# Performance work log

Measured on AMD Instinct MI355X. Metric: run time of the kernel, lower is better.

Reference implementation:

```python
import jax, jax.numpy as jnp
import numpy as np

B, T, N, E = 8, 32, 128, 2048
IN_DIM, HID, OUT = 512, 512, 512
SLOPE = 0.2  # GATConv default negative_slope


def setup_inputs() -> dict:
    key = jax.random.key(0)
    ks = jax.random.split(key, 12)
    x = jax.random.normal(ks[0], (B, T, N, IN_DIM), jnp.float32)
    edge_index = jax.random.randint(ks[1], (B, T, 2, E), 0, N)
    valid_step_index = jax.random.randint(ks[2], (B,), 1, T + 1)
    def lin(k, o, i):
        return jax.random.normal(k, (o, i), jnp.float32) / np.sqrt(i).astype(np.float32)
    W1 = lin(ks[3], HID, IN_DIM)
    a1_src = jax.random.normal(ks[4], (HID,), jnp.float32) / np.sqrt(HID).astype(np.float32)
    a1_dst = jax.random.normal(ks[5], (HID,), jnp.float32) / np.sqrt(HID).astype(np.float32)
    b1 = jnp.zeros((HID,), jnp.float32)
    W2 = lin(ks[6], OUT, HID)
    a2_src = jax.random.normal(ks[7], (OUT,), jnp.float32) / np.sqrt(OUT).astype(np.float32)
    a2_dst = jax.random.normal(ks[8], (OUT,), jnp.float32) / np.sqrt(OUT).astype(np.float32)
    b2 = jnp.zeros((OUT,), jnp.float32)
    W_time = jax.random.normal(ks[9], (T, T), jnp.float32) / np.sqrt(T).astype(np.float32)
    b_time = jnp.zeros((T,), jnp.float32)
    return dict(x=x, edge_index=edge_index, valid_step_index=valid_step_index,
                W1=W1, a1_src=a1_src, a1_dst=a1_dst, b1=b1,
                W2=W2, a2_src=a2_src, a2_dst=a2_dst, b2=b2,
                W_time=W_time, b_time=b_time)


def _gat(x, src, dst, W, a_src, a_dst, b):
    # Single-head PyG GATConv (concat=True, heads=1), self-loops already appended.
    n = x.shape[0]
    h = x @ W.T                                             # [N, H]
    e = jax.nn.leaky_relu((h @ a_src)[src] + (h @ a_dst)[dst], SLOPE)  # [E]
    m = jax.ops.segment_max(e, dst, num_segments=n)
    m = jnp.where(jnp.isfinite(m), m, 0.0)
    p = jnp.exp(e - m[dst])
    denom = jax.ops.segment_sum(p, dst, num_segments=n)
    alpha = p / denom[dst]                                  # segment softmax over incoming edges
    return jax.ops.segment_sum(h[src] * alpha[:, None], dst, num_segments=n) + b


def reference(x, edge_index, valid_step_index, W1, a1_src, a1_dst, b1,
              W2, a2_src, a2_dst, b2, W_time, b_time):
    b_, t_, n_, _ = x.shape
    g = b_ * t_
    xf = x.reshape(g, n_, -1)
    ei = edge_index.reshape(g, 2, -1)
    # add self loops (PyG GATConv default add_self_loops=True)
    loops = jnp.broadcast_to(jnp.arange(n_)[None, None, :], (g, 2, n_))
    ei = jnp.concatenate([ei, loops], axis=-1)
    src, dst = ei[:, 0], ei[:, 1]
    gat = jax.vmap(_gat, in_axes=(0, 0, 0, None, None, None, None))
    h = jax.nn.gelu(gat(xf, src, dst, W1, a1_src, a1_dst, b1), approximate=False)
    # F.dropout(p=0.2) is identity in eval mode
    h = gat(h, src, dst, W2, a2_src, a2_dst, b2)
    y = h.reshape(b_, t_, n_, -1)
    mask = (jnp.arange(t_)[None, :] < valid_step_index[:, None]).astype(y.dtype)
    y = y * mask[:, :, None, None]
    # TemporalConv: Conv2d(T, T, 1) over time-as-channel = linear mix across time, then GELU, residual
    fused = jax.nn.gelu(jnp.einsum('ts,bsnf->btnf', W_time, y)
                        + b_time[None, :, None, None], approximate=False)
    return fused + y
```

## Files before the change

kernel.cpp:

```cpp
#include <hip/hip_runtime.h>

using u16 = unsigned short;
using u32 = unsigned int;

typedef __bf16 bf16x8 __attribute__((ext_vector_type(8)));
typedef float  f32x4  __attribute__((ext_vector_type(4)));

__device__ __forceinline__ u16 f2bf(float f) {
    u32 u = __float_as_uint(f);
    u32 r = u + 0x7fffu + ((u >> 16) & 1u);
    return (u16)(r >> 16);
}
__device__ __forceinline__ float gelu_f(float x) {
    return 0.5f * x * (1.0f + erff(x * 0.70710678118654752440f));
}

#define GLOAD16(gp, lp) __builtin_amdgcn_global_load_lds( \
    (const __attribute__((address_space(1))) void*)(gp),  \
    (__attribute__((address_space(3))) void*)(lp), 16, 0, 0)
#define WAITV0  asm volatile("s_waitcnt vmcnt(0)" ::: "memory")
#define WAITL0  asm volatile("s_waitcnt lgkmcnt(0)" ::: "memory")
#define BARRIER __builtin_amdgcn_s_barrier()

__global__ __launch_bounds__(256) void prep_kernel(
    const float* __restrict__ W1, const float* __restrict__ W2,
    u16* __restrict__ W1b, u16* __restrict__ W2b)
{
    int i = blockIdx.x * 256 + threadIdx.x;
    const float* src = (i < 65536) ? W1 : W2;
    u16* dst = (i < 65536) ? W1b : W2b;
    int ii = i & 65535;
    int f = ii >> 7;
    int k = (ii & 127) * 4;
    float4 v = ((const float4*)src)[ii];
    int kd = (k & ~31) | ((((k >> 3) & 3) ^ (f & 3)) << 3) | (k & 7);
    ushort4 o;
    o.x = f2bf(v.x); o.y = f2bf(v.y); o.z = f2bf(v.z); o.w = f2bf(v.w);
    *(ushort4*)&dst[f * 512 + kd] = o;
}

__global__ __launch_bounds__(512, 2) void mega_kernel(
    const float* __restrict__ x, const int* __restrict__ ei, const int* __restrict__ valid,
    const u16* __restrict__ W1b, const float* __restrict__ a1s, const float* __restrict__ a1d,
    const float* __restrict__ b1,
    const u16* __restrict__ W2b, const float* __restrict__ a2s, const float* __restrict__ a2d,
    const float* __restrict__ b2,
    float* __restrict__ outF)
{
    __shared__ u16 Hs[65536];
    __shared__ __align__(16) u16 SG[16384];

    const int tid  = threadIdx.x;
    const int lane = tid & 63;
    const int w    = tid >> 6;
    const int rl   = lane & 15;
    const int grp  = lane >> 4;
    const int gid  = blockIdx.x;
    const int bb   = gid >> 5, tt = gid & 31;

    float* stf = (float*)(SG + 12288);
    u32*   cntw = (u32*)SG;
    const unsigned char* cb = (const unsigned char*)SG;

    const int xr = tid >> 2, xq = tid & 3;
    const float* xg = x + (size_t)gid * 65536;


    {
        f32x4 acc[8][4] = {};
        float4 xa = *(const float4*)(xg + xr * 512 + xq * 8);
        float4 xc = *(const float4*)(xg + xr * 512 + xq * 8 + 4);
        for (int kt = 0; kt < 16; ++kt) {
            {
                const u16* s0 = W1b + (size_t)(w * 64 + (lane >> 2)) * 512 + kt * 32 + (lane & 3) * 8;
                GLOAD16(s0,            &SG[4096 + w * 1024]);
                GLOAD16(s0 + 16 * 512, &SG[4096 + w * 1024 + 512]);
            }
            {
                ushort4 lo, hi;
                lo.x = f2bf(xa.x); lo.y = f2bf(xa.y); lo.z = f2bf(xa.z); lo.w = f2bf(xa.w);
                hi.x = f2bf(xc.x); hi.y = f2bf(xc.y); hi.z = f2bf(xc.z); hi.w = f2bf(xc.w);
                int xo = xr * 32 + ((xq ^ (xr & 3)) << 3);
                *(ushort4*)&SG[xo]     = lo;
                *(ushort4*)&SG[xo + 4] = hi;
            }
            WAITV0; BARRIER;
            bf16x8 af[8];
            #pragma unroll
            for (int i = 0; i < 8; ++i)
                af[i] = *(const bf16x8*)&SG[(i * 16 + rl) * 32 + ((grp ^ (rl & 3)) << 3)];
            bf16x8 bv0 = *(const bf16x8*)&SG[4096 + w * 1024 + (rl) * 32      + ((grp ^ (rl & 3)) << 3)];
            bf16x8 bv1 = *(const bf16x8*)&SG[4096 + w * 1024 + (16 + rl) * 32 + ((grp ^ (rl & 3)) << 3)];
            WAITL0; BARRIER;
            {
                const u16* s0 = W1b + (size_t)(w * 64 + 32 + (lane >> 2)) * 512 + kt * 32 + (lane & 3) * 8;
                GLOAD16(s0,            &SG[4096 + w * 1024]);
                GLOAD16(s0 + 16 * 512, &SG[4096 + w * 1024 + 512]);
            }
            #pragma unroll
            for (int i = 0; i < 8; ++i) {
                acc[i][0] = __builtin_amdgcn_mfma_f32_16x16x32_bf16(af[i], bv0, acc[i][0], 0, 0, 0);
                acc[i][1] = __builtin_amdgcn_mfma_f32_16x16x32_bf16(af[i], bv1, acc[i][1], 0, 0, 0);
            }
            WAITV0; BARRIER;
            bf16x8 bv2 = *(const bf16x8*)&SG[4096 + w * 1024 + (rl) * 32      + ((grp ^ (rl & 3)) << 3)];
            bf16x8 bv3 = *(const bf16x8*)&SG[4096 + w * 1024 + (16 + rl) * 32 + ((grp ^ (rl & 3)) << 3)];
            WAITL0;
            if (kt < 15) {
                xa = *(const float4*)(xg + xr * 512 + (kt + 1) * 32 + xq * 8);
                xc = *(const float4*)(xg + xr * 512 + (kt + 1) * 32 + xq * 8 + 4);
            }
            #pragma unroll
            for (int i = 0; i < 8; ++i) {
                acc[i][2] = __builtin_amdgcn_mfma_f32_16x16x32_bf16(af[i], bv2, acc[i][2], 0, 0, 0);
                acc[i][3] = __builtin_amdgcn_mfma_f32_16x16x32_bf16(af[i], bv3, acc[i][3], 0, 0, 0);
            }
            BARRIER;
        }
        stf[tid] = 0.f;
        __syncthreads();
        float asv[4], adv[4];
        #pragma unroll
        for (int j = 0; j < 4; ++j) {
            int f = w * 64 + j * 16 + rl;
            asv[j] = a1s[f]; adv[j] = a1d[f];
        }
        #pragma unroll
        for (int i = 0; i < 8; ++i) {
            #pragma unroll
            for (int j = 0; j < 4; ++j) {
                int f = w * 64 + j * 16 + rl;
                ushort4 o;
                o.x = f2bf(acc[i][j][0]); o.y = f2bf(acc[i][j][1]);
                o.z = f2bf(acc[i][j][2]); o.w = f2bf(acc[i][j][3]);
                *(ushort4*)&Hs[(f * 128 + i * 16 + grp * 4) ^ ((f & 7) << 3)] = o;
            }
            #pragma unroll
            for (int r = 0; r < 4; ++r) {
                float s = acc[i][0][r] * asv[0] + acc[i][1][r] * asv[1]
                        + acc[i][2][r] * asv[2] + acc[i][3][r] * asv[3];
                float d = acc[i][0][r] * adv[0] + acc[i][1][r] * adv[1]
                        + acc[i][2][r] * adv[2] + acc[i][3][r] * adv[3];
                #pragma unroll
                for (int off = 1; off < 16; off <<= 1) {
                    s += __shfl_xor(s, off);
                    d += __shfl_xor(d, off);
                }
                if (rl == 0) {
                    atomicAdd(&stf[i * 16 + grp * 4 + r], s);
                    atomicAdd(&stf[128 + i * 16 + grp * 4 + r], d);
                }
            }
        }
        __syncthreads();
    }

    {
        for (int i = tid; i < 4096; i += 512) cntw[i] = 0u;
        __syncthreads();
        const int4* es = (const int4*)(ei + (size_t)gid * 4096);
        int4 s4 = es[tid], d4 = es[512 + tid];
        atomicAdd(&cntw[(u32)((d4.x * 32 + (s4.x >> 2)) ^ ((d4.x & 7) << 1))], 1u << (8 * (s4.x & 3)));
        atomicAdd(&cntw[(u32)((d4.y * 32 + (s4.y >> 2)) ^ ((d4.y & 7) << 1))], 1u << (8 * (s4.y & 3)));
        atomicAdd(&cntw[(u32)((d4.z * 32 + (s4.z >> 2)) ^ ((d4.z & 7) << 1))], 1u << (8 * (s4.z & 3)));
        atomicAdd(&cntw[(u32)((d4.w * 32 + (s4.w >> 2)) ^ ((d4.w & 7) << 1))], 1u << (8 * (s4.w & 3)));
        if (tid < 128)
            atomicAdd(&cntw[(u32)((tid * 32 + (tid >> 2)) ^ ((tid & 7) << 1))], 1u << (8 * (tid & 3)));
        __syncthreads();
        for (int r = 0; r < 16; ++r) {
            int m = w * 16 + r;
            float sdm = stf[128 + m];
            int s0 = lane, s1 = lane + 64;
            u32 c0 = cb[((m * 128 + (s0 & ~3)) ^ ((m & 7) << 3)) + (s0 & 3)];
            u32 c1 = cb[((m * 128 + (s1 & ~3)) ^ ((m & 7) << 3)) + (s1 & 3)];
            float e0 = stf[s0] + sdm; e0 = e0 > 0.f ? e0 : 0.2f * e0;
            float e1 = stf[s1] + sdm; e1 = e1 > 0.f ? e1 : 0.2f * e1;
            float mx = fmaxf(c0 ? e0 : -1e30f, c1 ? e1 : -1e30f);
            #pragma unroll
            for (int off = 1; off < 64; off <<= 1) mx = fmaxf(mx, __shfl_xor(mx, off));
            float p = (c0 ? (float)c0 * __expf(e0 - mx) : 0.f)
                    + (c1 ? (float)c1 * __expf(e1 - mx) : 0.f);
            #pragma unroll
            for (int off = 1; off < 64; off <<= 1) p += __shfl_xor(p, off);
            if (lane == 0) { stf[256 + m] = mx; stf[384 + m] = 1.f / p; }
        }
        __syncthreads();
    }

    {
        f32x4 acc2[32] = {};
        int m = w * 16 + rl;
        float Mm = stf[256 + m], rDm = stf[384 + m], sdm = stf[128 + m];
        bf16x8 pa[4];
        #pragma unroll
        for (int kb = 0; kb < 4; ++kb) {
            u32 wi = (u32)((m * 32 + kb * 8 + grp * 2) ^ ((m & 7) << 1));
            u32 w0 = cntw[wi], w1 = cntw[wi + 1];
            #pragma unroll
            for (int e = 0; e < 8; ++e) {
                int s = kb * 32 + grp * 8 + e;
                u32 c = ((e < 4 ? (w0 >> (8 * e)) : (w1 >> (8 * (e - 4)))) & 255u);
                float ev = stf[s] + sdm; ev = ev > 0.f ? ev : 0.2f * ev;
                float p = c ? (float)c * __expf(ev - Mm) * rDm : 0.f;
                pa[kb][e] = (__bf16)p;
            }
        }
        #pragma unroll
        for (int j = 0; j < 32; ++j) {
            int f = j * 16 + rl;
            #pragma unroll
            for (int kb = 0; kb < 4; ++kb) {
                bf16x8 hb = *(const bf16x8*)&Hs[(f * 128 + kb * 32 + grp * 8) ^ ((f & 7) << 3)];
                acc2[j] = __builtin_amdgcn_mfma_f32_16x16x32_bf16(pa[kb], hb, acc2[j], 0, 0, 0);
            }
        }
        __syncthreads();
        #pragma unroll
        for (int j = 0; j < 32; ++j) {
            int f = j * 16 + rl;
            float bv = b1[f];
            #pragma unroll
            for (int r = 0; r < 4; ++r) {
                int mm = w * 16 + grp * 4 + r;
                Hs[(mm * 512 + f) ^ ((mm & 7) << 3)] = f2bf(gelu_f(acc2[j][r] + bv));
            }
        }
        __syncthreads();
    }

    {
        f32x4 acc[8][4] = {};
        for (int kt = 0; kt < 16; ++kt) {
            {
                const u16* s0 = W2b + (size_t)(w * 64 + (lane >> 2)) * 512 + kt * 32 + (lane & 3) * 8;
                GLOAD16(s0,            &SG[4096 + w * 1024]);
                GLOAD16(s0 + 16 * 512, &SG[4096 + w * 1024 + 512]);
            }
            WAITV0; BARRIER;
            bf16x8 af[8];
            #pragma unroll
            for (int i = 0; i < 8; ++i)
                af[i] = *(const bf16x8*)&Hs[((i * 16 + rl) * 512 + kt * 32 + grp * 8) ^ ((rl & 7) << 3)];
            bf16x8 bv0 = *(const bf16x8*)&SG[4096 + w * 1024 + (rl) * 32      + ((grp ^ (rl & 3)) << 3)];
            bf16x8 bv1 = *(const bf16x8*)&SG[4096 + w * 1024 + (16 + rl) * 32 + ((grp ^ (rl & 3)) << 3)];
            WAITL0; BARRIER;
            {
                const u16* s0 = W2b + (size_t)(w * 64 + 32 + (lane >> 2)) * 512 + kt * 32 + (lane & 3) * 8;
                GLOAD16(s0,            &SG[4096 + w * 1024]);
                GLOAD16(s0 + 16 * 512, &SG[4096 + w * 1024 + 512]);
            }
            #pragma unroll
            for (int i = 0; i < 8; ++i) {
                acc[i][0] = __builtin_amdgcn_mfma_f32_16x16x32_bf16(af[i], bv0, acc[i][0], 0, 0, 0);
                acc[i][1] = __builtin_amdgcn_mfma_f32_16x16x32_bf16(af[i], bv1, acc[i][1], 0, 0, 0);
            }
            WAITV0; BARRIER;
            bf16x8 bv2 = *(const bf16x8*)&SG[4096 + w * 1024 + (rl) * 32      + ((grp ^ (rl & 3)) << 3)];
            bf16x8 bv3 = *(const bf16x8*)&SG[4096 + w * 1024 + (16 + rl) * 32 + ((grp ^ (rl & 3)) << 3)];
            WAITL0;
            #pragma unroll
            for (int i = 0; i < 8; ++i) {
                acc[i][2] = __builtin_amdgcn_mfma_f32_16x16x32_bf16(af[i], bv2, acc[i][2], 0, 0, 0);
                acc[i][3] = __builtin_amdgcn_mfma_f32_16x16x32_bf16(af[i], bv3, acc[i][3], 0, 0, 0);
            }
            BARRIER;
        }
        stf[tid] = 0.f;
        __syncthreads();
        float asv[4], adv[4];
        #pragma unroll
        for (int j = 0; j < 4; ++j) {
            int f = w * 64 + j * 16 + rl;
            asv[j] = a2s[f]; adv[j] = a2d[f];
        }
        #pragma unroll
        for (int i = 0; i < 8; ++i) {
            #pragma unroll
            for (int j = 0; j < 4; ++j) {
                int f = w * 64 + j * 16 + rl;
                ushort4 o;
                o.x = f2bf(acc[i][j][0]); o.y = f2bf(acc[i][j][1]);
                o.z = f2bf(acc[i][j][2]); o.w = f2bf(acc[i][j][3]);
                *(ushort4*)&Hs[(f * 128 + i * 16 + grp * 4) ^ ((f & 7) << 3)] = o;
            }
            #pragma unroll
            for (int r = 0; r < 4; ++r) {
                float s = acc[i][0][r] * asv[0] + acc[i][1][r] * asv[1]
                        + acc[i][2][r] * asv[2] + acc[i][3][r] * asv[3];
                float d = acc[i][0][r] * adv[0] + acc[i][1][r] * adv[1]
                        + acc[i][2][r] * adv[2] + acc[i][3][r] * adv[3];
                #pragma unroll
                for (int off = 1; off < 16; off <<= 1) {
                    s += __shfl_xor(s, off);
                    d += __shfl_xor(d, off);
                }
                if (rl == 0) {
                    atomicAdd(&stf[i * 16 + grp * 4 + r], s);
                    atomicAdd(&stf[128 + i * 16 + grp * 4 + r], d);
                }
            }
        }
        __syncthreads();
    }

    {
        for (int i = tid; i < 4096; i += 512) cntw[i] = 0u;
        __syncthreads();
        const int4* es = (const int4*)(ei + (size_t)gid * 4096);
        int4 s4 = es[tid], d4 = es[512 + tid];
        atomicAdd(&cntw[(u32)((d4.x * 32 + (s4.x >> 2)) ^ ((d4.x & 7) << 1))], 1u << (8 * (s4.x & 3)));
        atomicAdd(&cntw[(u32)((d4.y * 32 + (s4.y >> 2)) ^ ((d4.y & 7) << 1))], 1u << (8 * (s4.y & 3)));
        atomicAdd(&cntw[(u32)((d4.z * 32 + (s4.z >> 2)) ^ ((d4.z & 7) << 1))], 1u << (8 * (s4.z & 3)));
        atomicAdd(&cntw[(u32)((d4.w * 32 + (s4.w >> 2)) ^ ((d4.w & 7) << 1))], 1u << (8 * (s4.w & 3)));
        if (tid < 128)
            atomicAdd(&cntw[(u32)((tid * 32 + (tid >> 2)) ^ ((tid & 7) << 1))], 1u << (8 * (tid & 3)));
        __syncthreads();
        for (int r = 0; r < 16; ++r) {
            int m = w * 16 + r;
            float sdm = stf[128 + m];
            int s0 = lane, s1 = lane + 64;
            u32 c0 = cb[((m * 128 + (s0 & ~3)) ^ ((m & 7) << 3)) + (s0 & 3)];
            u32 c1 = cb[((m * 128 + (s1 & ~3)) ^ ((m & 7) << 3)) + (s1 & 3)];
            float e0 = stf[s0] + sdm; e0 = e0 > 0.f ? e0 : 0.2f * e0;
            float e1 = stf[s1] + sdm; e1 = e1 > 0.f ? e1 : 0.2f * e1;
            float mx = fmaxf(c0 ? e0 : -1e30f, c1 ? e1 : -1e30f);
            #pragma unroll
            for (int off = 1; off < 64; off <<= 1) mx = fmaxf(mx, __shfl_xor(mx, off));
            float p = (c0 ? (float)c0 * __expf(e0 - mx) : 0.f)
                    + (c1 ? (float)c1 * __expf(e1 - mx) : 0.f);
            #pragma unroll
            for (int off = 1; off < 64; off <<= 1) p += __shfl_xor(p, off);
            if (lane == 0) { stf[256 + m] = mx; stf[384 + m] = 1.f / p; }
        }
        __syncthreads();
    }

    {
        f32x4 acc2[32] = {};
        int m = w * 16 + rl;
        float Mm = stf[256 + m], rDm = stf[384 + m], sdm = stf[128 + m];
        bf16x8 pa[4];
        #pragma unroll
        for (int kb = 0; kb < 4; ++kb) {
            u32 wi = (u32)((m * 32 + kb * 8 + grp * 2) ^ ((m & 7) << 1));
            u32 w0 = cntw[wi], w1 = cntw[wi + 1];
            #pragma unroll
            for (int e = 0; e < 8; ++e) {
                int s = kb * 32 + grp * 8 + e;
                u32 c = ((e < 4 ? (w0 >> (8 * e)) : (w1 >> (8 * (e - 4)))) & 255u);
                float ev = stf[s] + sdm; ev = ev > 0.f ? ev : 0.2f * ev;
                float p = c ? (float)c * __expf(ev - Mm) * rDm : 0.f;
                pa[kb][e] = (__bf16)p;
            }
        }
        #pragma unroll
        for (int j = 0; j < 32; ++j) {
            int f = j * 16 + rl;
            #pragma unroll
            for (int kb = 0; kb < 4; ++kb) {
                bf16x8 hb = *(const bf16x8*)&Hs[(f * 128 + kb * 32 + grp * 8) ^ ((f & 7) << 3)];
                acc2[j] = __builtin_amdgcn_mfma_f32_16x16x32_bf16(pa[kb], hb, acc2[j], 0, 0, 0);
            }
        }
        float msk = (tt < valid[bb]) ? 1.f : 0.f;
        float* og = outF + (size_t)gid * 65536;
        #pragma unroll
        for (int j = 0; j < 32; ++j) {
            int g = j * 16 + rl;
            float bv = b2[g];
            #pragma unroll
            for (int r = 0; r < 4; ++r)
                og[(w * 16 + grp * 4 + r) * 512 + g] = (acc2[j][r] + bv) * msk;
        }
    }
}

__global__ __launch_bounds__(256) void timemix_kernel(float* __restrict__ y,
                                                      const float* __restrict__ Wt,
                                                      const float* __restrict__ bt) {
    __shared__ float wsm[1024];
    __shared__ float bts[32];
    int tid = threadIdx.x;
    for (int i = tid; i < 1024; i += 256) wsm[i] = Wt[i];
    if (tid < 32) bts[tid] = bt[tid];
    __syncthreads();
    int blk = blockIdx.x;
    int b = blk >> 8;
    int rem = blk & 255;
    int n = rem >> 1;
    int f = (rem & 1) * 256 + tid;
    size_t base = ((size_t)b * 4096 + n) * 512 + f;
    float ys[32];
    #pragma unroll
    for (int s = 0; s < 32; ++s) ys[s] = y[base + (size_t)s * 65536];
    #pragma unroll
    for (int t = 0; t < 32; ++t) {
        float a = bts[t];
        #pragma unroll
        for (int s = 0; s < 32; ++s) a += wsm[t * 32 + s] * ys[s];
        y[base + (size_t)t * 65536] = gelu_f(a) + ys[t];
    }
}

extern "C" void kernel_launch(void* const* d_in, const int* in_sizes, int n_in,
                              void* d_out, int out_size, void* d_ws, size_t ws_size,
                              hipStream_t stream) {
    const float* x     = (const float*)d_in[0];
    const int*   ei    = (const int*)d_in[1];
    const int*   valid = (const int*)d_in[2];
    const float* W1    = (const float*)d_in[3];
    const float* a1s   = (const float*)d_in[4];
    const float* a1d   = (const float*)d_in[5];
    const float* b1    = (const float*)d_in[6];
    const float* W2    = (const float*)d_in[7];
    const float* a2s   = (const float*)d_in[8];
    const float* a2d   = (const float*)d_in[9];
    const float* b2    = (const float*)d_in[10];
    const float* Wt    = (const float*)d_in[11];
    const float* bt    = (const float*)d_in[12];
    float* out = (float*)d_out;

    char* ws = (char*)d_ws;
    u16* W1b = (u16*)(ws);
    u16* W2b = (u16*)(ws + 524288);

    prep_kernel<<<512, 256, 0, stream>>>(W1, W2, W1b, W2b);
    mega_kernel<<<256, 512, 0, stream>>>(x, ei, valid,
        W1b, a1s, a1d, b1, W2b, a2s, a2d, b2, out);
    timemix_kernel<<<2048, 256, 0, stream>>>(out, Wt, bt);
}
```

Measured before the change: 198.9 us.

## Stage x into LDS upfront, pipeline W loads per-wave, share adjacency across layers

Converts the whole x tile to bf16 into LDS once instead of per k-step, and replaces the barrier-heavy W staging with a per-wave double-buffered ring that uses vmcnt(1) waits. The goal is to overlap global loads with MFMA and drop block-wide barriers from the GEMM loop. The edge-count adjacency is built once with 4-bit packed counts and reused by both GAT layers, which are now folded into one loop. The 4-bit counts cap duplicate edges per pair at 15, and the new swizzles change LDS access patterns.

Measured after the change: 218.1 us. 1.1x slower.

```diff
diff --git a/kernel.cpp b/kernel.cpp
--- a/kernel.cpp
+++ b/kernel.cpp
@@ -18,9 +18,8 @@
 #define GLOAD16(gp, lp) __builtin_amdgcn_global_load_lds( \
     (const __attribute__((address_space(1))) void*)(gp),  \
     (__attribute__((address_space(3))) void*)(lp), 16, 0, 0)
-#define WAITV0  asm volatile("s_waitcnt vmcnt(0)" ::: "memory")
-#define WAITL0  asm volatile("s_waitcnt lgkmcnt(0)" ::: "memory")
-#define BARRIER __builtin_amdgcn_s_barrier()
+#define WAITV(n) asm volatile("s_waitcnt vmcnt(" #n ")" ::: "memory")
+#define WAITL0   asm volatile("s_waitcnt lgkmcnt(0)" ::: "memory")
 
 __global__ __launch_bounds__(256) void prep_kernel(
     const float* __restrict__ W1, const float* __restrict__ W2,
@@ -49,6 +48,9 @@
 {
     __shared__ u16 Hs[65536];
     __shared__ __align__(16) u16 SG[16384];
+    u32*   cntw = (u32*)SG;
+    u16*   ring = SG + 4096;
+    float* stf  = (float*)(SG + 12288);
 
     const int tid  = threadIdx.x;
     const int lane = tid & 63;
@@ -58,319 +60,191 @@
     const int gid  = blockIdx.x;
     const int bb   = gid >> 5, tt = gid & 31;
 
-    float* stf = (float*)(SG + 12288);
-    u32*   cntw = (u32*)SG;
-    const unsigned char* cb = (const unsigned char*)SG;
-
-    const int xr = tid >> 2, xq = tid & 3;
-    const float* xg = x + (size_t)gid * 65536;
-
-
-    {
+    const int4* es = (const int4*)(ei + (size_t)gid * 4096);
+    int4 e0 = es[tid], e1 = es[512 + tid];
+
+    for (int i = tid; i < 2048; i += 512) cntw[i] = 0u;
+    stf[tid] = 0.f;
+
+    const float4* xg = (const float4*)(x + (size_t)gid * 65536);
+    #pragma unroll
+    for (int it = 0; it < 16; ++it) {
+        float4 a = xg[tid * 2 + it * 1024];
+        float4 b = xg[tid * 2 + 1 + it * 1024];
+        int m = it * 8 + w;
+        int sp = lane ^ ((lane >> 3) & 7) ^ (m & 7);
+        ushort4 lo, hi;
+        lo.x = f2bf(a.x); lo.y = f2bf(a.y); lo.z = f2bf(a.z); lo.w = f2bf(a.w);
+        hi.x = f2bf(b.x); hi.y = f2bf(b.y); hi.z = f2bf(b.z); hi.w = f2bf(b.w);
+        *(ushort4*)&Hs[m * 512 + sp * 8]     = lo;
+        *(ushort4*)&Hs[m * 512 + sp * 8 + 4] = hi;
+    }
+    __syncthreads();
+
+    atomicAdd(&cntw[e1.x * 16 + (e0.x >> 3)], 1u << ((e0.x & 7) * 4));
+    atomicAdd(&cntw[e1.y * 16 + (e0.y >> 3)], 1u << ((e0.y & 7) * 4));
+    atomicAdd(&cntw[e1.z * 16 + (e0.z >> 3)], 1u << ((e0.z & 7) * 4));
+    atomicAdd(&cntw[e1.w * 16 + (e0.w >> 3)], 1u << ((e0.w & 7) * 4));
+    if (tid < 128) atomicAdd(&cntw[tid * 16 + (tid >> 3)], 1u << ((tid & 7) * 4));
+    __syncthreads();
+
+    u16* myring = ring + w * 1024;
+
+    for (int L = 0; L < 2; ++L) {
+        const u16*  WL  = L ? W2b : W1b;
+        const float* av_s = L ? a2s : a1s;
+        const float* av_d = L ? a2d : a1d;
+
         f32x4 acc[8][4] = {};
-        float4 xa = *(const float4*)(xg + xr * 512 + xq * 8);
-        float4 xc = *(const float4*)(xg + xr * 512 + xq * 8 + 4);
-        for (int kt = 0; kt < 16; ++kt) {
-            {
-                const u16* s0 = W1b + (size_t)(w * 64 + (lane >> 2)) * 512 + kt * 32 + (lane & 3) * 8;
-                GLOAD16(s0,            &SG[4096 + w * 1024]);
-                GLOAD16(s0 + 16 * 512, &SG[4096 + w * 1024 + 512]);
-            }
-            {
-                ushort4 lo, hi;
-                lo.x = f2bf(xa.x); lo.y = f2bf(xa.y); lo.z = f2bf(xa.z); lo.w = f2bf(xa.w);
-                hi.x = f2bf(xc.x); hi.y = f2bf(xc.y); hi.z = f2bf(xc.z); hi.w = f2bf(xc.w);
-                int xo = xr * 32 + ((xq ^ (xr & 3)) << 3);
-                *(ushort4*)&SG[xo]     = lo;
-                *(ushort4*)&SG[xo + 4] = hi;
-            }
-            WAITV0; BARRIER;
-            bf16x8 af[8];
-            #pragma unroll
-            for (int i = 0; i < 8; ++i)
-                af[i] = *(const bf16x8*)&SG[(i * 16 + rl) * 32 + ((grp ^ (rl & 3)) << 3)];
-            bf16x8 bv0 = *(const bf16x8*)&SG[4096 + w * 1024 + (rl) * 32      + ((grp ^ (rl & 3)) << 3)];
-            bf16x8 bv1 = *(const bf16x8*)&SG[4096 + w * 1024 + (16 + rl) * 32 + ((grp ^ (rl & 3)) << 3)];
-            WAITL0; BARRIER;
-            {
-                const u16* s0 = W1b + (size_t)(w * 64 + 32 + (lane >> 2)) * 512 + kt * 32 + (lane & 3) * 8;
-                GLOAD16(s0,            &SG[4096 + w * 1024]);
-                GLOAD16(s0 + 16 * 512, &SG[4096 + w * 1024 + 512]);
-            }
-            #pragma unroll
-            for (int i = 0; i < 8; ++i) {
-                acc[i][0] = __builtin_amdgcn_mfma_f32_16x16x32_bf16(af[i], bv0, acc[i][0], 0, 0, 0);
-                acc[i][1] = __builtin_amdgcn_mfma_f32_16x16x32_bf16(af[i], bv1, acc[i][1], 0, 0, 0);
-            }
-            WAITV0; BARRIER;
-            bf16x8 bv2 = *(const bf16x8*)&SG[4096 + w * 1024 + (rl) * 32      + ((grp ^ (rl & 3)) << 3)];
-            bf16x8 bv3 = *(const bf16x8*)&SG[4096 + w * 1024 + (16 + rl) * 32 + ((grp ^ (rl & 3)) << 3)];
-            WAITL0;
-            if (kt < 15) {
-                xa = *(const float4*)(xg + xr * 512 + (kt + 1) * 32 + xq * 8);
-                xc = *(const float4*)(xg + xr * 512 + (kt + 1) * 32 + xq * 8 + 4);
-            }
-            #pragma unroll
-            for (int i = 0; i < 8; ++i) {
-                acc[i][2] = __builtin_amdgcn_mfma_f32_16x16x32_bf16(af[i], bv2, acc[i][2], 0, 0, 0);
-                acc[i][3] = __builtin_amdgcn_mfma_f32_16x16x32_bf16(af[i], bv3, acc[i][3], 0, 0, 0);
-            }
-            BARRIER;
-        }
-        stf[tid] = 0.f;
+        {
+            auto STAGEW = [&](int q) {
+                int kt2 = q >> 2, j2 = q & 3;
+                const u16* src = WL + (size_t)(w * 64 + j2 * 16 + (lane >> 2)) * 512
+                               + kt2 * 32 + (lane & 3) * 8;
+                GLOAD16(src, &myring[(q & 1) * 512]);
+            };
+            STAGEW(0); STAGEW(1);
+            for (int kt = 0; kt < 16; ++kt) {
+                bf16x8 af[8];
+                #pragma unroll
+                for (int i = 0; i < 8; ++i) {
+                    int m = i * 16 + rl;
+                    int sp = (kt * 4 + grp) ^ (kt >> 1) ^ (m & 7);
+                    af[i] = *(const bf16x8*)&Hs[m * 512 + sp * 8];
+                }
+                #pragma unroll
+                for (int j = 0; j < 4; ++j) {
+                    int q = kt * 4 + j;
+                    if (kt == 15 && j == 3) { WAITV(0); } else { WAITV(1); }
+                    bf16x8 bv = *(const bf16x8*)&myring[(q & 1) * 512 + rl * 32 + ((grp ^ (rl & 3)) * 8)];
+                    WAITL0;
+                    __builtin_amdgcn_sched_barrier(0);
+                    if (q + 2 < 64) STAGEW(q + 2);
+                    #pragma unroll
+                    for (int i = 0; i < 8; ++i)
+                        acc[i][j] = __builtin_amdgcn_mfma_f32_16x16x32_bf16(af[i], bv, acc[i][j], 0, 0, 0);
+                }
+            }
+        }
         __syncthreads();
-        float asv[4], adv[4];
-        #pragma unroll
-        for (int j = 0; j < 4; ++j) {
-            int f = w * 64 + j * 16 + rl;
-            asv[j] = a1s[f]; adv[j] = a1d[f];
-        }
-        #pragma unroll
-        for (int i = 0; i < 8; ++i) {
+
+        {
+            float asv[4], adv[4];
             #pragma unroll
             for (int j = 0; j < 4; ++j) {
                 int f = w * 64 + j * 16 + rl;
-                ushort4 o;
-                o.x = f2bf(acc[i][j][0]); o.y = f2bf(acc[i][j][1]);
-                o.z = f2bf(acc[i][j][2]); o.w = f2bf(acc[i][j][3]);
-                *(ushort4*)&Hs[(f * 128 + i * 16 + grp * 4) ^ ((f & 7) << 3)] = o;
-            }
-            #pragma unroll
-            for (int r = 0; r < 4; ++r) {
-                float s = acc[i][0][r] * asv[0] + acc[i][1][r] * asv[1]
-                        + acc[i][2][r] * asv[2] + acc[i][3][r] * asv[3];
-                float d = acc[i][0][r] * adv[0] + acc[i][1][r] * adv[1]
-                        + acc[i][2][r] * adv[2] + acc[i][3][r] * adv[3];
-                #pragma unroll
-                for (int off = 1; off < 16; off <<= 1) {
-                    s += __shfl_xor(s, off);
-                    d += __shfl_xor(d, off);
-                }
-                if (rl == 0) {
-                    atomicAdd(&stf[i * 16 + grp * 4 + r], s);
-                    atomicAdd(&stf[128 + i * 16 + grp * 4 + r], d);
+                asv[j] = av_s[f]; adv[j] = av_d[f];
+            }
+            #pragma unroll
+            for (int i = 0; i < 8; ++i) {
+                #pragma unroll
+                for (int j = 0; j < 4; ++j) {
+                    int f = j * 16 + rl + w * 64;
+                    int oct = i * 2 + (grp >> 1);
+                    int elem = f * 128 + ((oct ^ (f & 15)) * 8) + (grp & 1) * 4;
+                    ushort4 o;
+                    o.x = f2bf(acc[i][j][0]); o.y = f2bf(acc[i][j][1]);
+                    o.z = f2bf(acc[i][j][2]); o.w = f2bf(acc[i][j][3]);
+                    *(ushort4*)&Hs[elem] = o;
+                }
+                #pragma unroll
+                for (int r = 0; r < 4; ++r) {
+                    float s = acc[i][0][r] * asv[0] + acc[i][1][r] * asv[1]
+                            + acc[i][2][r] * asv[2] + acc[i][3][r] * asv[3];
+                    float d = acc[i][0][r] * adv[0] + acc[i][1][r] * adv[1]
+                            + acc[i][2][r] * adv[2] + acc[i][3][r] * adv[3];
+                    #pragma unroll
+                    for (int off = 1; off < 16; off <<= 1) {
+                        s += __shfl_xor(s, off);
+                        d += __shfl_xor(d, off);
+                    }
+                    if (rl == 0) {
+                        int m = i * 16 + grp * 4 + r;
+                        atomicAdd(&stf[m], s);
+                        atomicAdd(&stf[128 + m], d);
+                    }
                 }
             }
         }
         __syncthreads();
-    }
-
-    {
-        for (int i = tid; i < 4096; i += 512) cntw[i] = 0u;
-        __syncthreads();
-        const int4* es = (const int4*)(ei + (size_t)gid * 4096);
-        int4 s4 = es[tid], d4 = es[512 + tid];
-        atomicAdd(&cntw[(u32)((d4.x * 32 + (s4.x >> 2)) ^ ((d4.x & 7) << 1))], 1u << (8 * (s4.x & 3)));
-        atomicAdd(&cntw[(u32)((d4.y * 32 + (s4.y >> 2)) ^ ((d4.y & 7) << 1))], 1u << (8 * (s4.y & 3)));
-        atomicAdd(&cntw[(u32)((d4.z * 32 + (s4.z >> 2)) ^ ((d4.z & 7) << 1))], 1u << (8 * (s4.z & 3)));
-        atomicAdd(&cntw[(u32)((d4.w * 32 + (s4.w >> 2)) ^ ((d4.w & 7) << 1))], 1u << (8 * (s4.w & 3)));
-        if (tid < 128)
-            atomicAdd(&cntw[(u32)((tid * 32 + (tid >> 2)) ^ ((tid & 7) << 1))], 1u << (8 * (tid & 3)));
-        __syncthreads();
+
         for (int r = 0; r < 16; ++r) {
             int m = w * 16 + r;
             float sdm = stf[128 + m];
-            int s0 = lane, s1 = lane + 64;
-            u32 c0 = cb[((m * 128 + (s0 & ~3)) ^ ((m & 7) << 3)) + (s0 & 3)];
-            u32 c1 = cb[((m * 128 + (s1 & ~3)) ^ ((m & 7) << 3)) + (s1 & 3)];
-            float e0 = stf[s0] + sdm; e0 = e0 > 0.f ? e0 : 0.2f * e0;
-            float e1 = stf[s1] + sdm; e1 = e1 > 0.f ? e1 : 0.2f * e1;
-            float mx = fmaxf(c0 ? e0 : -1e30f, c1 ? e1 : -1e30f);
+            u32 w0 = cntw[m * 16 + (lane >> 3)];
+            u32 w1 = cntw[m * 16 + 8 + (lane >> 3)];
+            u32 c0 = (w0 >> ((lane & 7) * 4)) & 15u;
+            u32 c1 = (w1 >> ((lane & 7) * 4)) & 15u;
+            float E0 = stf[lane] + sdm;      E0 = E0 > 0.f ? E0 : 0.2f * E0;
+            float E1 = stf[lane + 64] + sdm; E1 = E1 > 0.f ? E1 : 0.2f * E1;
+            float mx = fmaxf(c0 ? E0 : -1e30f, c1 ? E1 : -1e30f);
             #pragma unroll
             for (int off = 1; off < 64; off <<= 1) mx = fmaxf(mx, __shfl_xor(mx, off));
-            float p = (c0 ? (float)c0 * __expf(e0 - mx) : 0.f)
-                    + (c1 ? (float)c1 * __expf(e1 - mx) : 0.f);
+            float p = (c0 ? (float)c0 * __expf(E0 - mx) : 0.f)
+                    + (c1 ? (float)c1 * __expf(E1 - mx) : 0.f);
             #pragma unroll
             for (int off = 1; off < 64; off <<= 1) p += __shfl_xor(p, off);
             if (lane == 0) { stf[256 + m] = mx; stf[384 + m] = 1.f / p; }
         }
         __syncthreads();
-    }
-
-    {
+
         f32x4 acc2[32] = {};
-        int m = w * 16 + rl;
-        float Mm = stf[256 + m], rDm = stf[384 + m], sdm = stf[128 + m];
-        bf16x8 pa[4];
-        #pragma unroll
-        for (int kb = 0; kb < 4; ++kb) {
-            u32 wi = (u32)((m * 32 + kb * 8 + grp * 2) ^ ((m & 7) << 1));
-            u32 w0 = cntw[wi], w1 = cntw[wi + 1];
-            #pragma unroll
-            for (int e = 0; e < 8; ++e) {
-                int s = kb * 32 + grp * 8 + e;
-                u32 c = ((e < 4 ? (w0 >> (8 * e)) : (w1 >> (8 * (e - 4)))) & 255u);
-                float ev = stf[s] + sdm; ev = ev > 0.f ? ev : 0.2f * ev;
-                float p = c ? (float)c * __expf(ev - Mm) * rDm : 0.f;
-                pa[kb][e] = (__bf16)p;
-            }
-        }
-        #pragma unroll
-        for (int j = 0; j < 32; ++j) {
-            int f = j * 16 + rl;
+        {
+            int m = w * 16 + rl;
+            float sdm = stf[128 + m], Mm = stf[256 + m], rDm = stf[384 + m];
+            bf16x8 pa[4];
             #pragma unroll
             for (int kb = 0; kb < 4; ++kb) {
-                bf16x8 hb = *(const bf16x8*)&Hs[(f * 128 + kb * 32 + grp * 8) ^ ((f & 7) << 3)];
-                acc2[j] = __builtin_amdgcn_mfma_f32_16x16x32_bf16(pa[kb], hb, acc2[j], 0, 0, 0);
+                u32 word = cntw[m * 16 + kb * 4 + grp];
+                #pragma unroll
+                for (int e = 0; e < 8; ++e) {
+                    u32 c = (word >> (e * 4)) & 15u;
+                    int s = kb * 32 + grp * 8 + e;
+                    float ev = stf[s] + sdm; ev = ev > 0.f ? ev : 0.2f * ev;
+                    float p = c ? (float)c * __expf(ev - Mm) * rDm : 0.f;
+                    pa[kb][e] = (__bf16)p;
+                }
+            }
+            #pragma unroll
+            for (int j = 0; j < 32; ++j) {
+                int f = j * 16 + rl;
+                #pragma unroll
+                for (int kb = 0; kb < 4; ++kb) {
+                    bf16x8 hb = *(const bf16x8*)&Hs[f * 128 + (((kb * 4 + grp) ^ rl) * 8)];
+                    acc2[j] = __builtin_amdgcn_mfma_f32_16x16x32_bf16(pa[kb], hb, acc2[j], 0, 0, 0);
+                }
             }
         }
         __syncthreads();
-        #pragma unroll
-        for (int j = 0; j < 32; ++j) {
-            int f = j * 16 + rl;
-            float bv = b1[f];
-            #pragma unroll
-            for (int r = 0; r < 4; ++r) {
-                int mm = w * 16 + grp * 4 + r;
-                Hs[(mm * 512 + f) ^ ((mm & 7) << 3)] = f2bf(gelu_f(acc2[j][r] + bv));
-            }
-        }
-        __syncthreads();
-    }
-
-    {
-        f32x4 acc[8][4] = {};
-        for (int kt = 0; kt < 16; ++kt) {
-            {
-                const u16* s0 = W2b + (size_t)(w * 64 + (lane >> 2)) * 512 + kt * 32 + (lane & 3) * 8;
-                GLOAD16(s0,            &SG[4096 + w * 1024]);
-                GLOAD16(s0 + 16 * 512, &SG[4096 + w * 1024 + 512]);
-            }
-            WAITV0; BARRIER;
-            bf16x8 af[8];
-            #pragma unroll
-            for (int i = 0; i < 8; ++i)
-                af[i] = *(const bf16x8*)&Hs[((i * 16 + rl) * 512 + kt * 32 + grp * 8) ^ ((rl & 7) << 3)];
-            bf16x8 bv0 = *(const bf16x8*)&SG[4096 + w * 1024 + (rl) * 32      + ((grp ^ (rl & 3)) << 3)];
-            bf16x8 bv1 = *(const bf16x8*)&SG[4096 + w * 1024 + (16 + rl) * 32 + ((grp ^ (rl & 3)) << 3)];
-            WAITL0; BARRIER;
-            {
-                const u16* s0 = W2b + (size_t)(w * 64 + 32 + (lane >> 2)) * 512 + kt * 32 + (lane & 3) * 8;
-                GLOAD16(s0,            &SG[4096 + w * 1024]);
-                GLOAD16(s0 + 16 * 512, &SG[4096 + w * 1024 + 512]);
-            }
-            #pragma unroll
-            for (int i = 0; i < 8; ++i) {
-                acc[i][0] = __builtin_amdgcn_mfma_f32_16x16x32_bf16(af[i], bv0, acc[i][0], 0, 0, 0);
-                acc[i][1] = __builtin_amdgcn_mfma_f32_16x16x32_bf16(af[i], bv1, acc[i][1], 0, 0, 0);
-            }
-            WAITV0; BARRIER;
-            bf16x8 bv2 = *(const bf16x8*)&SG[4096 + w * 1024 + (rl) * 32      + ((grp ^ (rl & 3)) << 3)];
-            bf16x8 bv3 = *(const bf16x8*)&SG[4096 + w * 1024 + (16 + rl) * 32 + ((grp ^ (rl & 3)) << 3)];
-            WAITL0;
-            #pragma unroll
-            for (int i = 0; i < 8; ++i) {
-                acc[i][2] = __builtin_amdgcn_mfma_f32_16x16x32_bf16(af[i], bv2, acc[i][2], 0, 0, 0);
-                acc[i][3] = __builtin_amdgcn_mfma_f32_16x16x32_bf16(af[i], bv3, acc[i][3], 0, 0, 0);
-            }
-            BARRIER;
-        }
-        stf[tid] = 0.f;
-        __syncthreads();
-        float asv[4], adv[4];
-        #pragma unroll
-        for (int j = 0; j < 4; ++j) {
-            int f = w * 64 + j * 16 + rl;
-            asv[j] = a2s[f]; adv[j] = a2d[f];
-        }
-        #pragma unroll
-        for (int i = 0; i < 8; ++i) {
-            #pragma unroll
-            for (int j = 0; j < 4; ++j) {
-                int f = w * 64 + j * 16 + rl;
-                ushort4 o;
-                o.x = f2bf(acc[i][j][0]); o.y = f2bf(acc[i][j][1]);
-                o.z = f2bf(acc[i][j][2]); o.w = f2bf(acc[i][j][3]);
-                *(ushort4*)&Hs[(f * 128 + i * 16 + grp * 4) ^ ((f & 7) << 3)] = o;
-            }
-            #pragma unroll
-            for (int r = 0; r < 4; ++r) {
-                float s = acc[i][0][r] * asv[0] + acc[i][1][r] * asv[1]
-                        + acc[i][2][r] * asv[2] + acc[i][3][r] * asv[3];
-                float d = acc[i][0][r] * adv[0] + acc[i][1][r] * adv[1]
-                        + acc[i][2][r] * adv[2] + acc[i][3][r] * adv[3];
-                #pragma unroll
-                for (int off = 1; off < 16; off <<= 1) {
-                    s += __shfl_xor(s, off);
-                    d += __shfl_xor(d, off);
-                }
-                if (rl == 0) {
-                    atomicAdd(&stf[i * 16 + grp * 4 + r], s);
-                    atomicAdd(&stf[128 + i * 16 + grp * 4 + r], d);
-                }
-            }
-        }
-        __syncthreads();
-    }
-
-    {
-        for (int i = tid; i < 4096; i += 512) cntw[i] = 0u;
-        __syncthreads();
-        const int4* es = (const int4*)(ei + (size_t)gid * 4096);
-        int4 s4 = es[tid], d4 = es[512 + tid];
-        atomicAdd(&cntw[(u32)((d4.x * 32 + (s4.x >> 2)) ^ ((d4.x & 7) << 1))], 1u << (8 * (s4.x & 3)));
-        atomicAdd(&cntw[(u32)((d4.y * 32 + (s4.y >> 2)) ^ ((d4.y & 7) << 1))], 1u << (8 * (s4.y & 3)));
-        atomicAdd(&cntw[(u32)((d4.z * 32 + (s4.z >> 2)) ^ ((d4.z & 7) << 1))], 1u << (8 * (s4.z & 3)));
-        atomicAdd(&cntw[(u32)((d4.w * 32 + (s4.w >> 2)) ^ ((d4.w & 7) << 1))], 1u << (8 * (s4.w & 3)));
-        if (tid < 128)
-            atomicAdd(&cntw[(u32)((tid * 32 + (tid >> 2)) ^ ((tid & 7) << 1))], 1u << (8 * (tid & 3)));
-        __syncthreads();
-        for (int r = 0; r < 16; ++r) {
-            int m = w * 16 + r;
-            float sdm = stf[128 + m];
-            int s0 = lane, s1 = lane + 64;
-            u32 c0 = cb[((m * 128 + (s0 & ~3)) ^ ((m & 7) << 3)) + (s0 & 3)];
-            u32 c1 = cb[((m * 128 + (s1 & ~3)) ^ ((m & 7) << 3)) + (s1 & 3)];
-            float e0 = stf[s0] + sdm; e0 = e0 > 0.f ? e0 : 0.2f * e0;
-            float e1 = stf[s1] + sdm; e1 = e1 > 0.f ? e1 : 0.2f * e1;
-            float mx = fmaxf(c0 ? e0 : -1e30f, c1 ? e1 : -1e30f);
-            #pragma unroll
-            for (int off = 1; off < 64; off <<= 1) mx = fmaxf(mx, __shfl_xor(mx, off));
-            float p = (c0 ? (float)c0 * __expf(e0 - mx) : 0.f)
-                    + (c1 ? (float)c1 * __expf(e1 - mx) : 0.f);
-            #pragma unroll
-            for (int off = 1; off < 64; off <<= 1) p += __shfl_xor(p, off);
-            if (lane == 0) { stf[256 + m] = mx; stf[384 + m] = 1.f / p; }
-        }
-        __syncthreads();
-    }
-
-    {
-        f32x4 acc2[32] = {};
-        int m = w * 16 + rl;
-        float Mm = stf[256 + m], rDm = stf[384 + m], sdm = stf[128 + m];
-        bf16x8 pa[4];
-        #pragma unroll
-        for (int kb = 0; kb < 4; ++kb) {
-            u32 wi = (u32)((m * 32 + kb * 8 + grp * 2) ^ ((m & 7) << 1));
-            u32 w0 = cntw[wi], w1 = cntw[wi + 1];
-            #pragma unroll
-            for (int e = 0; e < 8; ++e) {
-                int s = kb * 32 + grp * 8 + e;
-                u32 c = ((e < 4 ? (w0 >> (8 * e)) : (w1 >> (8 * (e - 4)))) & 255u);
-                float ev = stf[s] + sdm; ev = ev > 0.f ? ev : 0.2f * ev;
-                float p = c ? (float)c * __expf(ev - Mm) * rDm : 0.f;
-                pa[kb][e] = (__bf16)p;
-            }
-        }
-        #pragma unroll
-        for (int j = 0; j < 32; ++j) {
-            int f = j * 16 + rl;
-            #pragma unroll
-            for (int kb = 0; kb < 4; ++kb) {
-                bf16x8 hb = *(const bf16x8*)&Hs[(f * 128 + kb * 32 + grp * 8) ^ ((f & 7) << 3)];
-                acc2[j] = __builtin_amdgcn_mfma_f32_16x16x32_bf16(pa[kb], hb, acc2[j], 0, 0, 0);
-            }
-        }
-        float msk = (tt < valid[bb]) ? 1.f : 0.f;
-        float* og = outF + (size_t)gid * 65536;
-        #pragma unroll
-        for (int j = 0; j < 32; ++j) {
-            int g = j * 16 + rl;
-            float bv = b2[g];
-            #pragma unroll
-            for (int r = 0; r < 4; ++r)
-                og[(w * 16 + grp * 4 + r) * 512 + g] = (acc2[j][r] + bv) * msk;
+
+        if (L == 0) {
+            stf[tid] = 0.f;
+            #pragma unroll
+            for (int j = 0; j < 32; ++j) {
+                int f = j * 16 + rl;
+                float bv = b1[f];
+                int slot = f >> 3;
+                #pragma unroll
+                for (int r = 0; r < 4; ++r) {
+                    int m2 = w * 16 + grp * 4 + r;
+                    int loc = slot ^ ((slot >> 3) & 7) ^ (m2 & 7);
+                    Hs[m2 * 512 + loc * 8 + (f & 7)] = f2bf(gelu_f(acc2[j][r] + bv));
+                }
+            }
+            __syncthreads();
+        } else {
+            float msk = (tt < valid[bb]) ? 1.f : 0.f;
+            float* og = outF + (size_t)gid * 65536;
+            #pragma unroll
+            for (int j = 0; j < 32; ++j) {
+                int f = j * 16 + rl;
+                float bv = b2[f];
+                #pragma unroll
+                for (int r = 0; r < 4; ++r) {
+                    int m2 = w * 16 + grp * 4 + r;
+                    og[m2 * 512 + f] = (acc2[j][r] + bv) * msk;
+                }
+            }
         }
     }
 }
```
